# Performance work log

Hardware: AMD Instinct MI355X
Metric: run time of the kernel (lower is better)

The kernel has to match this reference:

```python
import jax, jax.numpy as jnp
import numpy as np

THRESHOLD = 0.5

def setup_inputs() -> dict:
    key = jax.random.key(0)
    k1, k2 = jax.random.split(key)
    N, F, B = 800000, 64, 8
    xs = jax.random.uniform(k1, (N, 1), dtype=jnp.float32)          # scores in [0,1)
    pl = jax.random.normal(k2, (N, F), dtype=jnp.float32)           # payload features
    rs = (jnp.arange(B + 1, dtype=jnp.int32) * (N // B))            # row splits [0,100k,...,800k]
    return {"xs": xs, "pl": pl, "rs": rs}

def reference(xs, pl, rs):
    # SelectThreshold(xs, pl, rs, threshold=0.5):
    #   keep rows with score > threshold, compact features, recompute row splits,
    #   and emit scatter indices (original row ids of the kept rows).
    # JIT-static variant: kept rows are stably compacted to the front of an
    # [N, F] buffer; slots >= n_sel are zero-padded, scatter idx padded with N.
    N = pl.shape[0]
    B = rs.shape[0] - 1
    mask = xs[:, 0] > THRESHOLD                                      # [N] bool
    # stable argsort: selected rows first, original (per-segment) order preserved
    order = jnp.argsort(jnp.logical_not(mask))                       # [N] int
    n_sel = jnp.sum(mask.astype(jnp.int32))
    valid = jnp.arange(N) < n_sel                                    # [N] bool
    newfeat = jnp.where(valid[:, None], pl[order], jnp.zeros((), pl.dtype))  # [N, F]
    scatter_idxs = jnp.where(valid, order, N).astype(jnp.int32)[:, None]     # [N, 1]
    # per-event selected counts -> new row splits
    seg_ids = jnp.searchsorted(rs, jnp.arange(N, dtype=rs.dtype), side='right') - 1  # [N]
    counts = jax.ops.segment_sum(mask.astype(rs.dtype), seg_ids, num_segments=B)     # [B]
    new_rs = jnp.concatenate([jnp.zeros((1,), rs.dtype), jnp.cumsum(counts)])        # [B+1]
    return newfeat, new_rs, scatter_idxs
```

## Files before the change

kernel.cpp:

```cpp
#include <hip/hip_runtime.h>


#define THRESH 0.5f
#define RPB 1024

__global__ void k_count(const float* __restrict__ xs, int N,
                        int* __restrict__ ranks, int* __restrict__ blk_counts) {
    __shared__ int wc[4][4];
    const int tid  = threadIdx.x;
    const int lane = tid & 63, wave = tid >> 6;
    const int base = blockIdx.x * RPB;
    int running = 0;
    for (int c = 0; c < 4; ++c) {
        int i = base + c * 256 + tid;
        int m = (i < N) && (xs[i] > THRESH);
        unsigned long long bal = __ballot(m);
        if (lane == 0) wc[c][wave] = __popcll(bal);
        __syncthreads();
        int waveoff = 0, tot = 0;
        for (int w = 0; w < 4; ++w) { int v = wc[c][w]; if (w < wave) waveoff += v; tot += v; }
        int pre = running + waveoff + (int)__popcll(bal & ((1ull << lane) - 1ull));
        if (i < N) ranks[i] = (pre << 1) | m;
        running += tot;
    }
    if (tid == 0) blk_counts[blockIdx.x] = running;
}

__global__ void k_scan(const int* __restrict__ blk_counts, int nblocks,
                       const int* __restrict__ ranks,
                       const int* __restrict__ rs, int nrs, int N,
                       int* __restrict__ blk_off, int* __restrict__ nsel_out,
                       float* __restrict__ out_rs) {
    __shared__ int s[1024];
    __shared__ int s_total;
    const int t = threadIdx.x;
    int v = (t < nblocks) ? blk_counts[t] : 0;
    s[t] = v;
    __syncthreads();
    for (int d = 1; d < 1024; d <<= 1) {
        int add = (t >= d) ? s[t - d] : 0;
        __syncthreads();
        s[t] += add;
        __syncthreads();
    }
    int excl = s[t] - v;
    if (t < nblocks) blk_off[t] = excl;
    if (t == 1023) s_total = s[t];
    __syncthreads();
    int n_sel = s_total;
    if (t == 0) nsel_out[0] = n_sel;
    if (t < nrs) {
        int j = rs[t];
        int val;
        if (j >= N)      val = n_sel;
        else if (j <= 0) val = 0;
        else             val = blk_off[j >> 10] + (ranks[j] >> 1);
        out_rs[t] = (float)val;
    }
}

__global__ void k_scatter(const int* __restrict__ ranks, const int* __restrict__ blk_off,
                          const int* __restrict__ nsel, int N,
                          float* __restrict__ out_sc) {
    int i = blockIdx.x * blockDim.x + threadIdx.x;
    if (i >= N) return;
    int ns = nsel[0];
    int e  = ranks[i];
    if (e & 1) {
        int r = blk_off[i >> 10] + (e >> 1);
        out_sc[r] = (float)i;
    }
    if (i >= ns) out_sc[i] = (float)N;
}

__global__ void k_gather(const float* __restrict__ out_sc, const float4* __restrict__ pl4,
                         int N, float4* __restrict__ outf4) {
    int tid = blockIdx.x * blockDim.x + threadIdx.x;
    int r = tid >> 4;
    int c = tid & 15;
    if (r >= N) return;
    int idx = (int)out_sc[r];
    float4 v = make_float4(0.f, 0.f, 0.f, 0.f);
    if (idx < N) v = pl4[(size_t)idx * 16 + c];
    outf4[(size_t)r * 16 + c] = v;
}

extern "C" void kernel_launch(void* const* d_in, const int* in_sizes, int n_in,
                              void* d_out, int out_size, void* d_ws, size_t ws_size,
                              hipStream_t stream) {
    const float* xs = (const float*)d_in[0];
    const float* pl = (const float*)d_in[1];
    const int*   rs = (const int*)d_in[2];
    const int N   = in_sizes[0];
    const int F   = in_sizes[1] / N;
    const int nrs = in_sizes[2];

    float* out      = (float*)d_out;
    float* out_feat = out;
    float* out_rs   = out + (size_t)N * F;
    float* out_sc   = out_rs + nrs;

    int* ranks      = (int*)d_ws;
    int* blk_counts = ranks + N;
    int* blk_off    = blk_counts + 1024;
    int* nsel       = blk_off + 1024;

    const int nblocks = (N + RPB - 1) / RPB;

    k_count  <<<nblocks,           256,  0, stream>>>(xs, N, ranks, blk_counts);
    k_scan   <<<1,                 1024, 0, stream>>>(blk_counts, nblocks, ranks, rs, nrs, N,
                                                      blk_off, nsel, out_rs);
    k_scatter<<<(N + 255) / 256,   256,  0, stream>>>(ranks, blk_off, nsel, N, out_sc);
    k_gather <<<(N * (F / 4) + 255) / 256, 256, 0, stream>>>(out_sc, (const float4*)pl,
                                                             N, (float4*)out_feat);
}
```

Baseline: 343.3 us.

## Fuse scatter and gather into one push-style scatter-gather kernel

Replaces the separate scatter-index kernel and the pull-style gather kernel with one kernel. Each source row reads its payload coalesced and writes it to its compacted destination, and rows at or past n_sel are zero-filled in the same pass. This removes one launch and the round trip of the scatter indices through global memory before the gather. In exchange, writes become scattered by row, though each 256-byte row write stays contiguous.

```diff
diff --git a/kernel.cpp b/kernel.cpp
--- a/kernel.cpp
+++ b/kernel.cpp
@@ -59,30 +59,28 @@
     }
 }
 
-__global__ void k_scatter(const int* __restrict__ ranks, const int* __restrict__ blk_off,
-                          const int* __restrict__ nsel, int N,
-                          float* __restrict__ out_sc) {
-    int i = blockIdx.x * blockDim.x + threadIdx.x;
+__global__ void k_scatter_gather(const int* __restrict__ ranks,
+                                 const int* __restrict__ blk_off,
+                                 const int* __restrict__ nsel,
+                                 const float4* __restrict__ pl4, int N,
+                                 float4* __restrict__ outf4,
+                                 float* __restrict__ out_sc) {
+    int tid = blockIdx.x * blockDim.x + threadIdx.x;
+    int i = tid >> 4;
+    int c = tid & 15;
     if (i >= N) return;
-    int ns = nsel[0];
-    int e  = ranks[i];
+    const int ns = nsel[0];
+    const int e  = ranks[i];
     if (e & 1) {
         int r = blk_off[i >> 10] + (e >> 1);
-        out_sc[r] = (float)i;
+        float4 v = pl4[(size_t)i * 16 + c];
+        outf4[(size_t)r * 16 + c] = v;
+        if (c == 0) out_sc[r] = (float)i;
     }
-    if (i >= ns) out_sc[i] = (float)N;
-}
-
-__global__ void k_gather(const float* __restrict__ out_sc, const float4* __restrict__ pl4,
-                         int N, float4* __restrict__ outf4) {
-    int tid = blockIdx.x * blockDim.x + threadIdx.x;
-    int r = tid >> 4;
-    int c = tid & 15;
-    if (r >= N) return;
-    int idx = (int)out_sc[r];
-    float4 v = make_float4(0.f, 0.f, 0.f, 0.f);
-    if (idx < N) v = pl4[(size_t)idx * 16 + c];
-    outf4[(size_t)r * 16 + c] = v;
+    if (i >= ns) {
+        outf4[(size_t)i * 16 + c] = make_float4(0.f, 0.f, 0.f, 0.f);
+        if (c == 0) out_sc[i] = (float)N;
+    }
 }
 
 extern "C" void kernel_launch(void* const* d_in, const int* in_sizes, int n_in,
@@ -107,10 +105,9 @@
 
     const int nblocks = (N + RPB - 1) / RPB;
 
-    k_count  <<<nblocks,           256,  0, stream>>>(xs, N, ranks, blk_counts);
-    k_scan   <<<1,                 1024, 0, stream>>>(blk_counts, nblocks, ranks, rs, nrs, N,
-                                                      blk_off, nsel, out_rs);
-    k_scatter<<<(N + 255) / 256,   256,  0, stream>>>(ranks, blk_off, nsel, N, out_sc);
-    k_gather <<<(N * (F / 4) + 255) / 256, 256, 0, stream>>>(out_sc, (const float4*)pl,
-                                                             N, (float4*)out_feat);
+    k_count<<<nblocks, 256, 0, stream>>>(xs, N, ranks, blk_counts);
+    k_scan <<<1,       1024, 0, stream>>>(blk_counts, nblocks, ranks, rs, nrs, N,
+                                          blk_off, nsel, out_rs);
+    k_scatter_gather<<<(N * 16 + 255) / 256, 256, 0, stream>>>(
+        ranks, blk_off, nsel, (const float4*)pl, N, (float4*)out_feat, out_sc);
 }
```

After: 343.3 us (median of 2 runs). Within noise of the previous version (-0.0%).
